# Kernel tuning notes

Measured on AMD Instinct MI355X. Metric: run time of the kernel, lower is better.

Reference implementation:

```python
import jax, jax.numpy as jnp
import numpy as np

MAX_WORDS = 256  # = batch['labels'].shape[1]


def _align(hidden, word_ids, max_words):
    """Batched segment-mean: (B,S,D) subtoken states -> (B,max_words,D) word states.
    Equivalent to align_subtokens_to_words applied per sample (word_ids all valid)."""
    B, S, D = hidden.shape
    seg = (word_ids.astype(jnp.int32) + jnp.arange(B, dtype=jnp.int32)[:, None] * max_words).reshape(-1)
    sums = jax.ops.segment_sum(hidden.reshape(-1, D), seg, num_segments=B * max_words)
    cnts = jax.ops.segment_sum(jnp.ones((B * S,), hidden.dtype), seg, num_segments=B * max_words)
    out = jnp.where(cnts[:, None] > 0, sums / jnp.maximum(cnts, 1.0)[:, None], 0.0)
    return out.reshape(B, max_words, D)


def setup_inputs() -> dict:
    key = jax.random.key(0)
    ks = jax.random.split(key, 8)
    B, S, D, W = 64, 512, 768, MAX_WORDS
    h_hing_sub = jax.random.normal(ks[0], (B, S, D), dtype=jnp.float32)
    h_rob_sub = jax.random.normal(ks[1], (B, S, D), dtype=jnp.float32)
    hing_word_ids = jnp.sort(jax.random.randint(ks[2], (B, S), 0, W), axis=-1).astype(jnp.int32)
    rob_word_ids = jnp.sort(jax.random.randint(ks[3], (B, S), 0, W), axis=-1).astype(jnp.int32)
    num_words = jax.random.randint(ks[4], (B,), 1, W).astype(jnp.int32)
    router_w1 = jax.random.normal(ks[5], (2 * D, 256), dtype=jnp.float32) * (1.0 / np.sqrt(2 * D))
    router_b1 = jnp.zeros((256,), jnp.float32)
    router_w2 = jax.random.normal(ks[6], (256, 1), dtype=jnp.float32) * (1.0 / 16.0)
    router_b2 = jnp.zeros((1,), jnp.float32)
    head_w = jax.random.normal(ks[7], (D, 7), dtype=jnp.float32) * (1.0 / np.sqrt(D))
    head_b = jnp.zeros((7,), jnp.float32)
    return {
        'h_hing_sub': h_hing_sub, 'h_rob_sub': h_rob_sub,
        'hing_word_ids': hing_word_ids, 'rob_word_ids': rob_word_ids,
        'num_words': num_words,
        'router_w1': router_w1, 'router_b1': router_b1,
        'router_w2': router_w2, 'router_b2': router_b2,
        'head_w': head_w, 'head_b': head_b,
    }


def reference(h_hing_sub, h_rob_sub, hing_word_ids, rob_word_ids, num_words,
              router_w1, router_b1, router_w2, router_b2, head_w, head_b):
    W = MAX_WORDS
    # scatter-mean subtokens -> words (the dominant custom-kernel op)
    h_hing = _align(h_hing_sub, hing_word_ids, W)   # (B, W, 768)
    h_rob = _align(h_rob_sub, rob_word_ids, W)      # (B, W, 768)
    # token-level MLP router on concatenated word states (router_input='both')
    router_in = jnp.concatenate([h_hing, h_rob], axis=-1)             # (B, W, 1536)
    hdn = jax.nn.relu(jnp.einsum('bwd,dh->bwh', router_in, router_w1) + router_b1)
    alpha = jax.nn.sigmoid(jnp.einsum('bwh,ho->bwo', hdn, router_w2) + router_b2)  # (B, W, 1)
    blended = alpha * h_hing + (1.0 - alpha) * h_rob                  # (B, W, 768)
    logits = jnp.einsum('bwd,dl->bwl', blended, head_w) + head_b      # (B, W, num_labels)
    l2_disagreement = jnp.linalg.norm(h_hing - h_rob, axis=-1)        # (B, W)
    return logits, alpha.squeeze(-1), l2_disagreement
```

## Files before the change

### kernel.cpp

```cpp
#include <hip/hip_runtime.h>
#include <hip/hip_bf16.h>
#include <math.h>

#define BATCH 64
#define SEQ   512
#define DIM   768
#define NW    256
#define NT    (BATCH * NW)
#define KDIM  1536
#define HID   256
#define NL    7

#define BM  32
#define BK  64
#define BKP 72
#define NKT (KDIM / BK)

typedef __bf16 bf16_t;
typedef bf16_t bf16x4 __attribute__((ext_vector_type(4)));
typedef bf16_t bf16x8 __attribute__((ext_vector_type(8)));
typedef float  f32x4  __attribute__((ext_vector_type(4)));

__global__ __launch_bounds__(256) void prep_kernel(
    const float* __restrict__ w1, bf16_t* __restrict__ w1t,
    const int* __restrict__ idh, const int* __restrict__ idr,
    int* __restrict__ starts)
{
    if (blockIdx.x < 192) {
        int kc = blockIdx.x >> 3;
        int kg = blockIdx.x & 7;
        int n  = threadIdx.x;
        bf16x8 v;
        #pragma unroll
        for (int j = 0; j < 8; j++)
            v[j] = (bf16_t)w1[(size_t)(kc * 64 + kg * 8 + j) * HID + n];
        *(bf16x8*)(w1t + (size_t)kc * (HID * BK) + n * BK + kg * 8) = v;
    } else {
        int blk = blockIdx.x - 192;
        int t = blk >> 6;
        int b = blk & 63;
        const int* ids = (t ? idr : idh) + b * SEQ;
        int w = threadIdx.x;
        int lo = 0, hi = SEQ;
        while (lo < hi) {
            int m = (lo + hi) >> 1;
            if (ids[m] < w) lo = m + 1; else hi = m;
        }
        int* row = starts + blk * 257;
        row[w] = lo;
        if (w == 0) row[256] = SEQ;
    }
}

__global__ __launch_bounds__(256) void align_kernel(
    const float* __restrict__ hh, const float* __restrict__ hr,
    const int* __restrict__ starts, bf16_t* __restrict__ X)
{
    int idx  = blockIdx.x * 256 + threadIdx.x;
    int rest = idx / 192;
    int c    = idx - rest * 192;
    rest     = __builtin_amdgcn_readfirstlane(rest);
    int w    = rest & 255;
    int t    = (rest >> 8) & 1;
    int b    = rest >> 9;

    const int* st = starts + (t * 64 + b) * 257;
    int lo = st[w];
    int hi = st[w + 1];

    const f32x4* src = (const f32x4*)((t ? hr : hh) + (size_t)b * SEQ * DIM);
    bf16_t*      dst = X + (size_t)b * NW * KDIM + (size_t)w * KDIM
                         + t * DIM + c * 4;

    bf16x4 o = {};
    int n = hi - lo;
    if (n > 0) {
        f32x4 acc = src[(size_t)lo * 192 + c];
        for (int s = lo + 1; s < hi; s++) {
            f32x4 v = src[(size_t)s * 192 + c];
            acc[0] += v[0]; acc[1] += v[1];
            acc[2] += v[2]; acc[3] += v[3];
        }
        float inv = 1.0f / (float)n;
        o[0] = (bf16_t)(acc[0] * inv);
        o[1] = (bf16_t)(acc[1] * inv);
        o[2] = (bf16_t)(acc[2] * inv);
        o[3] = (bf16_t)(acc[3] * inv);
    }
    *(bf16x4*)dst = o;
}

__global__ __launch_bounds__(256) void gemm_alpha_kernel(
    const bf16_t* __restrict__ X, const bf16_t* __restrict__ w1t,
    const float* __restrict__ b1, const float* __restrict__ w2,
    const float* __restrict__ b2, float* __restrict__ out)
{
    __shared__ __align__(16) bf16_t Xs[BM][BKP];
    __shared__ __align__(16) bf16_t Ws[HID][BKP];
    __shared__ float alpha_acc[BM];

    int tid   = threadIdx.x;
    int lane  = tid & 63;
    int wv    = tid >> 6;
    int row16 = lane & 15;
    int quad  = lane >> 4;
    int tok0  = blockIdx.x * BM;

    f32x4 acc[2][4];
    #pragma unroll
    for (int mi = 0; mi < 2; mi++)
        #pragma unroll
        for (int ni = 0; ni < 4; ni++)
            acc[mi][ni] = (f32x4){0.f, 0.f, 0.f, 0.f};

    int xr = tid >> 3;
    int xc = tid & 7;

    for (int kc = 0; kc < NKT; kc++) {
        {
            const uint4* src = (const uint4*)(X + (size_t)(tok0 + xr) * KDIM + kc * BK + xc * 8);
            *(uint4*)(&Xs[xr][xc * 8]) = *src;
        }
        {
            const uint4* srcb = (const uint4*)(w1t + (size_t)kc * (HID * BK));
            #pragma unroll
            for (int i = 0; i < 8; i++) {
                int cidx = tid + i * 256;
                *(uint4*)(&Ws[cidx >> 3][(cidx & 7) * 8]) = srcb[cidx];
            }
        }
        __syncthreads();
        #pragma unroll
        for (int kk2 = 0; kk2 < 2; kk2++) {
            bf16x8 af[2], bfg[4];
            #pragma unroll
            for (int mi = 0; mi < 2; mi++)
                af[mi] = *(const bf16x8*)(&Xs[mi * 16 + row16][kk2 * 32 + quad * 8]);
            #pragma unroll
            for (int ni = 0; ni < 4; ni++)
                bfg[ni] = *(const bf16x8*)(&Ws[wv * 64 + ni * 16 + row16][kk2 * 32 + quad * 8]);
            #pragma unroll
            for (int mi = 0; mi < 2; mi++)
                #pragma unroll
                for (int ni = 0; ni < 4; ni++)
                    acc[mi][ni] = __builtin_amdgcn_mfma_f32_16x16x32_bf16(
                        af[mi], bfg[ni], acc[mi][ni], 0, 0, 0);
        }
        __syncthreads();
    }

    float w2v[4], b1v[4];
    #pragma unroll
    for (int ni = 0; ni < 4; ni++) {
        int col = wv * 64 + ni * 16 + row16;
        w2v[ni] = w2[col];
        b1v[ni] = b1[col];
    }
    if (tid < BM) alpha_acc[tid] = 0.f;
    __syncthreads();

    #pragma unroll
    for (int mi = 0; mi < 2; mi++) {
        #pragma unroll
        for (int r = 0; r < 4; r++) {
            float p = 0.f;
            #pragma unroll
            for (int ni = 0; ni < 4; ni++) {
                float v = acc[mi][ni][r] + b1v[ni];
                v = v > 0.f ? v : 0.f;
                p += v * w2v[ni];
            }
            p += __shfl_xor(p, 1);
            p += __shfl_xor(p, 2);
            p += __shfl_xor(p, 4);
            p += __shfl_xor(p, 8);
            if (row16 == 0)
                atomicAdd(&alpha_acc[mi * 16 + quad * 4 + r], p);
        }
    }
    __syncthreads();
    if (tid < BM) {
        float a = 1.f / (1.f + expf(-(alpha_acc[tid] + b2[0])));
        out[(size_t)NT * NL + tok0 + tid] = a;
    }
}

__global__ __launch_bounds__(256) void blend_kernel(
    const bf16_t* __restrict__ X, const float* __restrict__ hw,
    const float* __restrict__ hb, float* __restrict__ out)
{
    __shared__ float hws[NL * DIM];
    int tid  = threadIdx.x;
    int lane = tid & 63;
    int wv   = tid >> 6;

    for (int i = tid; i < DIM * NL; i += 256) {
        int d = i / NL, l = i - d * NL;
        hws[l * DIM + d] = hw[i];
    }
    __syncthreads();

    int g   = lane >> 3;
    int u   = lane & 7;
    int tok = blockIdx.x * 32 + wv * 8 + g;

    float a = out[(size_t)NT * NL + tok];
    const bf16_t* xrow = X + (size_t)tok * KDIM;

    float lg[NL] = {0.f, 0.f, 0.f, 0.f, 0.f, 0.f, 0.f};
    float l2 = 0.f;

    #pragma unroll
    for (int k = 0; k < 12; k++) {
        int d0 = (k * 8 + u) * 8;
        bf16x8 hp = *(const bf16x8*)(xrow + d0);
        bf16x8 rp = *(const bf16x8*)(xrow + DIM + d0);
        float bl[8];
        #pragma unroll
        for (int e = 0; e < 8; e++) {
            float hhv = (float)hp[e];
            float hrv = (float)rp[e];
            float df  = hhv - hrv;
            bl[e] = fmaf(a, df, hrv);
            l2 = fmaf(df, df, l2);
        }
        #pragma unroll
        for (int l = 0; l < NL; l++) {
            f32x4 wA = *(const f32x4*)(&hws[l * DIM + d0]);
            f32x4 wB = *(const f32x4*)(&hws[l * DIM + d0 + 4]);
            lg[l] += bl[0]*wA[0] + bl[1]*wA[1] + bl[2]*wA[2] + bl[3]*wA[3]
                   + bl[4]*wB[0] + bl[5]*wB[1] + bl[6]*wB[2] + bl[7]*wB[3];
        }
    }

    #pragma unroll
    for (int off = 1; off < 8; off <<= 1) {
        #pragma unroll
        for (int l = 0; l < NL; l++) lg[l] += __shfl_xor(lg[l], off);
        l2 += __shfl_xor(l2, off);
    }

    if (u < NL) {
        float v = (u == 0) ? lg[0] : (u == 1) ? lg[1] : (u == 2) ? lg[2]
                : (u == 3) ? lg[3] : (u == 4) ? lg[4] : (u == 5) ? lg[5] : lg[6];
        out[(size_t)tok * NL + u] = v + hb[u];
    } else {
        out[(size_t)NT * NL + NT + tok] = sqrtf(l2);
    }
}

extern "C" void kernel_launch(void* const* d_in, const int* in_sizes, int n_in,
                              void* d_out, int out_size, void* d_ws, size_t ws_size,
                              hipStream_t stream)
{
    const float* hh  = (const float*)d_in[0];
    const float* hr  = (const float*)d_in[1];
    const int*   idh = (const int*)d_in[2];
    const int*   idr = (const int*)d_in[3];
    const float* w1  = (const float*)d_in[5];
    const float* b1  = (const float*)d_in[6];
    const float* w2  = (const float*)d_in[7];
    const float* b2  = (const float*)d_in[8];
    const float* hw  = (const float*)d_in[9];
    const float* hb  = (const float*)d_in[10];
    float* out = (float*)d_out;

    bf16_t* X      = (bf16_t*)d_ws;
    bf16_t* w1t    = X + (size_t)NT * KDIM;
    int*    starts = (int*)(w1t + (size_t)NKT * HID * BK);

    prep_kernel<<<320, 256, 0, stream>>>(w1, w1t, idh, idr, starts);
    align_kernel<<<24576, 256, 0, stream>>>(hh, hr, starts, X);
    gemm_alpha_kernel<<<NT / BM, 256, 0, stream>>>(X, w1t, b1, w2, b2, out);
    blend_kernel<<<512, 256, 0, stream>>>(X, hw, hb, out);
}
```

Before: 279.8 us.

## Fuse align, router GEMM and blend into one kernel with LDS-resident word states

Merges the segment-mean align, the router MLP GEMM and the blend/logits/L2 stage into a single kernel. Each 512-thread block handles 16 words of one batch row and keeps their bf16 word states in shared memory, so the intermediate X buffer no longer makes a global round trip. The GEMM now reads W1 fragments straight from global/L2 instead of staging them in LDS. In exchange there are only 1024 blocks, a 16-row MFMA tile, and the per-word 7x768 head-weight transpose is recomputed in every block, which may hurt latency hiding.

```diff
diff --git a/kernel.cpp b/kernel.cpp
--- a/kernel.cpp
+++ b/kernel.cpp
@@ -10,11 +10,12 @@
 #define KDIM  1536
 #define HID   256
 #define NL    7
-
-#define BM  32
-#define BK  64
-#define BKP 72
-#define NKT (KDIM / BK)
+#define BK    64
+#define NKT   (KDIM / BK)
+
+#define TPB   512
+#define TPW   16
+#define XSP   1544
 
 typedef __bf16 bf16_t;
 typedef bf16_t bf16x4 __attribute__((ext_vector_type(4)));
@@ -52,200 +53,148 @@
     }
 }
 
-__global__ __launch_bounds__(256) void align_kernel(
+__global__ __launch_bounds__(TPB, 4) void fused_kernel(
     const float* __restrict__ hh, const float* __restrict__ hr,
-    const int* __restrict__ starts, bf16_t* __restrict__ X)
+    const int* __restrict__ starts, const bf16_t* __restrict__ w1t,
+    const float* __restrict__ b1, const float* __restrict__ w2,
+    const float* __restrict__ b2, const float* __restrict__ hw,
+    const float* __restrict__ hb, float* __restrict__ out)
 {
-    int idx  = blockIdx.x * 256 + threadIdx.x;
-    int rest = idx / 192;
-    int c    = idx - rest * 192;
-    rest     = __builtin_amdgcn_readfirstlane(rest);
-    int w    = rest & 255;
-    int t    = (rest >> 8) & 1;
-    int b    = rest >> 9;
-
-    const int* st = starts + (t * 64 + b) * 257;
-    int lo = st[w];
-    int hi = st[w + 1];
-
-    const f32x4* src = (const f32x4*)((t ? hr : hh) + (size_t)b * SEQ * DIM);
-    bf16_t*      dst = X + (size_t)b * NW * KDIM + (size_t)w * KDIM
-                         + t * DIM + c * 4;
-
-    bf16x4 o = {};
-    int n = hi - lo;
-    if (n > 0) {
-        f32x4 acc = src[(size_t)lo * 192 + c];
-        for (int s = lo + 1; s < hi; s++) {
-            f32x4 v = src[(size_t)s * 192 + c];
-            acc[0] += v[0]; acc[1] += v[1];
-            acc[2] += v[2]; acc[3] += v[3];
-        }
-        float inv = 1.0f / (float)n;
-        o[0] = (bf16_t)(acc[0] * inv);
-        o[1] = (bf16_t)(acc[1] * inv);
-        o[2] = (bf16_t)(acc[2] * inv);
-        o[3] = (bf16_t)(acc[3] * inv);
-    }
-    *(bf16x4*)dst = o;
-}
-
-__global__ __launch_bounds__(256) void gemm_alpha_kernel(
-    const bf16_t* __restrict__ X, const bf16_t* __restrict__ w1t,
-    const float* __restrict__ b1, const float* __restrict__ w2,
-    const float* __restrict__ b2, float* __restrict__ out)
-{
-    __shared__ __align__(16) bf16_t Xs[BM][BKP];
-    __shared__ __align__(16) bf16_t Ws[HID][BKP];
-    __shared__ float alpha_acc[BM];
-
-    int tid   = threadIdx.x;
-    int lane  = tid & 63;
-    int wv    = tid >> 6;
+    __shared__ __align__(16) bf16_t Xs[TPW][XSP];
+    __shared__ float hws[NL * DIM];
+    __shared__ float alpha_acc[TPW];
+    __shared__ float alpha_s[TPW];
+
+    int tid  = threadIdx.x;
+    int lane = tid & 63;
+    int wv   = tid >> 6;
+    int b    = blockIdx.x >> 4;
+    int wb   = blockIdx.x & 15;
+    int tok0 = b * NW + wb * TPW;
+
+    for (int i = tid; i < DIM * NL; i += TPB) {
+        int d = i / NL, l = i - d * NL;
+        hws[l * DIM + d] = hw[i];
+    }
+    if (tid < TPW) alpha_acc[tid] = 0.f;
+
+    #pragma unroll
+    for (int wi = 0; wi < 2; wi++) {
+        int wl = wv * 2 + wi;
+        int w  = wb * TPW + wl;
+        #pragma unroll
+        for (int tt = 0; tt < 2; tt++) {
+            const int* st = starts + (tt * 64 + b) * 257;
+            int lo = __builtin_amdgcn_readfirstlane(st[w]);
+            int n  = __builtin_amdgcn_readfirstlane(st[w + 1]) - lo;
+            const f32x4* src = (const f32x4*)((tt ? hr : hh)
+                                + (size_t)b * SEQ * DIM) + lane;
+            f32x4 a0 = {0.f,0.f,0.f,0.f}, a1 = a0, a2 = a0;
+            for (int s = lo; s < lo + n; s++) {
+                const f32x4* r = src + (size_t)s * 192;
+                a0 += r[0]; a1 += r[64]; a2 += r[128];
+            }
+            float inv = n > 0 ? 1.0f / (float)n : 0.0f;
+            bf16x4 o0, o1, o2;
+            #pragma unroll
+            for (int e = 0; e < 4; e++) {
+                o0[e] = (bf16_t)(a0[e] * inv);
+                o1[e] = (bf16_t)(a1[e] * inv);
+                o2[e] = (bf16_t)(a2[e] * inv);
+            }
+            bf16_t* xr = &Xs[wl][tt * DIM];
+            *(bf16x4*)(xr + lane * 4)         = o0;
+            *(bf16x4*)(xr + (lane + 64) * 4)  = o1;
+            *(bf16x4*)(xr + (lane + 128) * 4) = o2;
+        }
+    }
+    __syncthreads();
+
     int row16 = lane & 15;
     int quad  = lane >> 4;
-    int tok0  = blockIdx.x * BM;
-
-    f32x4 acc[2][4];
-    #pragma unroll
-    for (int mi = 0; mi < 2; mi++)
-        #pragma unroll
-        for (int ni = 0; ni < 4; ni++)
-            acc[mi][ni] = (f32x4){0.f, 0.f, 0.f, 0.f};
-
-    int xr = tid >> 3;
-    int xc = tid & 7;
-
-    for (int kc = 0; kc < NKT; kc++) {
-        {
-            const uint4* src = (const uint4*)(X + (size_t)(tok0 + xr) * KDIM + kc * BK + xc * 8);
-            *(uint4*)(&Xs[xr][xc * 8]) = *src;
-        }
-        {
-            const uint4* srcb = (const uint4*)(w1t + (size_t)kc * (HID * BK));
-            #pragma unroll
-            for (int i = 0; i < 8; i++) {
-                int cidx = tid + i * 256;
-                *(uint4*)(&Ws[cidx >> 3][(cidx & 7) * 8]) = srcb[cidx];
-            }
-        }
-        __syncthreads();
-        #pragma unroll
-        for (int kk2 = 0; kk2 < 2; kk2++) {
-            bf16x8 af[2], bfg[4];
-            #pragma unroll
-            for (int mi = 0; mi < 2; mi++)
-                af[mi] = *(const bf16x8*)(&Xs[mi * 16 + row16][kk2 * 32 + quad * 8]);
-            #pragma unroll
-            for (int ni = 0; ni < 4; ni++)
-                bfg[ni] = *(const bf16x8*)(&Ws[wv * 64 + ni * 16 + row16][kk2 * 32 + quad * 8]);
-            #pragma unroll
-            for (int mi = 0; mi < 2; mi++)
-                #pragma unroll
-                for (int ni = 0; ni < 4; ni++)
-                    acc[mi][ni] = __builtin_amdgcn_mfma_f32_16x16x32_bf16(
-                        af[mi], bfg[ni], acc[mi][ni], 0, 0, 0);
-        }
-        __syncthreads();
-    }
-
-    float w2v[4], b1v[4];
-    #pragma unroll
-    for (int ni = 0; ni < 4; ni++) {
-        int col = wv * 64 + ni * 16 + row16;
-        w2v[ni] = w2[col];
-        b1v[ni] = b1[col];
-    }
-    if (tid < BM) alpha_acc[tid] = 0.f;
-    __syncthreads();
-
-    #pragma unroll
-    for (int mi = 0; mi < 2; mi++) {
+    f32x4 acc0 = {0.f,0.f,0.f,0.f}, acc1 = acc0;
+    int col0 = wv * 32 + row16;
+    #pragma unroll 2
+    for (int ks = 0; ks < 48; ks++) {
+        int kc = ks >> 1, k2 = ks & 1;
+        bf16x8 af = *(const bf16x8*)(&Xs[row16][ks * 32 + quad * 8]);
+        const bf16_t* bp = w1t + (size_t)kc * (HID * BK) + k2 * 32 + quad * 8;
+        bf16x8 bf0 = *(const bf16x8*)(bp + (size_t)col0 * BK);
+        bf16x8 bf1 = *(const bf16x8*)(bp + (size_t)(col0 + 16) * BK);
+        acc0 = __builtin_amdgcn_mfma_f32_16x16x32_bf16(af, bf0, acc0, 0, 0, 0);
+        acc1 = __builtin_amdgcn_mfma_f32_16x16x32_bf16(af, bf1, acc1, 0, 0, 0);
+    }
+
+    {
+        float w2v0 = w2[col0],     b1v0 = b1[col0];
+        float w2v1 = w2[col0 + 16], b1v1 = b1[col0 + 16];
         #pragma unroll
         for (int r = 0; r < 4; r++) {
-            float p = 0.f;
-            #pragma unroll
-            for (int ni = 0; ni < 4; ni++) {
-                float v = acc[mi][ni][r] + b1v[ni];
-                v = v > 0.f ? v : 0.f;
-                p += v * w2v[ni];
-            }
+            float v0 = acc0[r] + b1v0; v0 = v0 > 0.f ? v0 : 0.f;
+            float v1 = acc1[r] + b1v1; v1 = v1 > 0.f ? v1 : 0.f;
+            float p = v0 * w2v0 + v1 * w2v1;
             p += __shfl_xor(p, 1);
             p += __shfl_xor(p, 2);
             p += __shfl_xor(p, 4);
             p += __shfl_xor(p, 8);
             if (row16 == 0)
-                atomicAdd(&alpha_acc[mi * 16 + quad * 4 + r], p);
+                atomicAdd(&alpha_acc[quad * 4 + r], p);
         }
     }
     __syncthreads();
-    if (tid < BM) {
+    if (tid < TPW) {
         float a = 1.f / (1.f + expf(-(alpha_acc[tid] + b2[0])));
+        alpha_s[tid] = a;
         out[(size_t)NT * NL + tok0 + tid] = a;
     }
-}
-
-__global__ __launch_bounds__(256) void blend_kernel(
-    const bf16_t* __restrict__ X, const float* __restrict__ hw,
-    const float* __restrict__ hb, float* __restrict__ out)
-{
-    __shared__ float hws[NL * DIM];
-    int tid  = threadIdx.x;
-    int lane = tid & 63;
-    int wv   = tid >> 6;
-
-    for (int i = tid; i < DIM * NL; i += 256) {
-        int d = i / NL, l = i - d * NL;
-        hws[l * DIM + d] = hw[i];
-    }
     __syncthreads();
 
-    int g   = lane >> 3;
-    int u   = lane & 7;
-    int tok = blockIdx.x * 32 + wv * 8 + g;
-
-    float a = out[(size_t)NT * NL + tok];
-    const bf16_t* xrow = X + (size_t)tok * KDIM;
-
-    float lg[NL] = {0.f, 0.f, 0.f, 0.f, 0.f, 0.f, 0.f};
-    float l2 = 0.f;
-
-    #pragma unroll
-    for (int k = 0; k < 12; k++) {
-        int d0 = (k * 8 + u) * 8;
-        bf16x8 hp = *(const bf16x8*)(xrow + d0);
-        bf16x8 rp = *(const bf16x8*)(xrow + DIM + d0);
-        float bl[8];
-        #pragma unroll
-        for (int e = 0; e < 8; e++) {
-            float hhv = (float)hp[e];
-            float hrv = (float)rp[e];
-            float df  = hhv - hrv;
-            bl[e] = fmaf(a, df, hrv);
-            l2 = fmaf(df, df, l2);
-        }
-        #pragma unroll
-        for (int l = 0; l < NL; l++) {
-            f32x4 wA = *(const f32x4*)(&hws[l * DIM + d0]);
-            f32x4 wB = *(const f32x4*)(&hws[l * DIM + d0 + 4]);
-            lg[l] += bl[0]*wA[0] + bl[1]*wA[1] + bl[2]*wA[2] + bl[3]*wA[3]
-                   + bl[4]*wB[0] + bl[5]*wB[1] + bl[6]*wB[2] + bl[7]*wB[3];
-        }
-    }
-
-    #pragma unroll
-    for (int off = 1; off < 8; off <<= 1) {
-        #pragma unroll
-        for (int l = 0; l < NL; l++) lg[l] += __shfl_xor(lg[l], off);
-        l2 += __shfl_xor(l2, off);
-    }
-
-    if (u < NL) {
-        float v = (u == 0) ? lg[0] : (u == 1) ? lg[1] : (u == 2) ? lg[2]
-                : (u == 3) ? lg[3] : (u == 4) ? lg[4] : (u == 5) ? lg[5] : lg[6];
-        out[(size_t)tok * NL + u] = v + hb[u];
-    } else {
-        out[(size_t)NT * NL + NT + tok] = sqrtf(l2);
+    {
+        int tl = wv * 2 + (lane >> 5);
+        int u  = lane & 31;
+        float a = alpha_s[tl];
+
+        float lg[NL] = {0.f, 0.f, 0.f, 0.f, 0.f, 0.f, 0.f};
+        float l2 = 0.f;
+
+        #pragma unroll
+        for (int g3 = 0; g3 < 3; g3++) {
+            int d0 = u * 24 + g3 * 8;
+            bf16x8 hp = *(const bf16x8*)(&Xs[tl][d0]);
+            bf16x8 rp = *(const bf16x8*)(&Xs[tl][DIM + d0]);
+            float bl[8];
+            #pragma unroll
+            for (int e = 0; e < 8; e++) {
+                float hhv = (float)hp[e];
+                float hrv = (float)rp[e];
+                float df  = hhv - hrv;
+                bl[e] = fmaf(a, df, hrv);
+                l2 = fmaf(df, df, l2);
+            }
+            #pragma unroll
+            for (int l = 0; l < NL; l++) {
+                f32x4 wA = *(const f32x4*)(&hws[l * DIM + d0]);
+                f32x4 wB = *(const f32x4*)(&hws[l * DIM + d0 + 4]);
+                lg[l] += bl[0]*wA[0] + bl[1]*wA[1] + bl[2]*wA[2] + bl[3]*wA[3]
+                       + bl[4]*wB[0] + bl[5]*wB[1] + bl[6]*wB[2] + bl[7]*wB[3];
+            }
+        }
+
+        #pragma unroll
+        for (int off = 1; off < 32; off <<= 1) {
+            #pragma unroll
+            for (int l = 0; l < NL; l++) lg[l] += __shfl_xor(lg[l], off);
+            l2 += __shfl_xor(l2, off);
+        }
+
+        int tok = tok0 + tl;
+        if (u < NL) {
+            float v = (u == 0) ? lg[0] : (u == 1) ? lg[1] : (u == 2) ? lg[2]
+                    : (u == 3) ? lg[3] : (u == 4) ? lg[4] : (u == 5) ? lg[5] : lg[6];
+            out[(size_t)tok * NL + u] = v + hb[u];
+        } else if (u == NL) {
+            out[(size_t)NT * NL + NT + tok] = sqrtf(l2);
+        }
     }
 }
 
@@ -265,12 +214,10 @@
     const float* hb  = (const float*)d_in[10];
     float* out = (float*)d_out;
 
-    bf16_t* X      = (bf16_t*)d_ws;
-    bf16_t* w1t    = X + (size_t)NT * KDIM;
+    bf16_t* w1t    = (bf16_t*)d_ws;
     int*    starts = (int*)(w1t + (size_t)NKT * HID * BK);
 
     prep_kernel<<<320, 256, 0, stream>>>(w1, w1t, idh, idr, starts);
-    align_kernel<<<24576, 256, 0, stream>>>(hh, hr, starts, X);
-    gemm_alpha_kernel<<<NT / BM, 256, 0, stream>>>(X, w1t, b1, w2, b2, out);
-    blend_kernel<<<512, 256, 0, stream>>>(X, hw, hb, out);
+    fused_kernel<<<BATCH * 16, TPB, 0, stream>>>(hh, hr, starts, w1t,
+                                                 b1, w2, b2, hw, hb, out);
 }
```

After: 335.3 us. 19.8% more time.

## Fuse blend into GEMM epilogue and give each wave one word in align

Applied to the files above, without the earlier changes.

The blend/logits/L2 kernel is merged into the router GEMM kernel. It reuses the weight-tile shared memory for the head weights and keeps alpha in shared memory, which removes one launch and the global round-trip of alpha. The align kernel is restructured so each wavefront handles one (batch, type, word) row, with three f32x4 accumulators per lane and wave-uniform segment bounds. This replaces the earlier per-thread division indexing and cuts the block count. The extra smem staging of the head weights adds latency to the GEMM tail.

```diff
diff --git a/kernel.cpp b/kernel.cpp
--- a/kernel.cpp
+++ b/kernel.cpp
@@ -56,48 +56,55 @@
     const float* __restrict__ hh, const float* __restrict__ hr,
     const int* __restrict__ starts, bf16_t* __restrict__ X)
 {
-    int idx  = blockIdx.x * 256 + threadIdx.x;
-    int rest = idx / 192;
-    int c    = idx - rest * 192;
-    rest     = __builtin_amdgcn_readfirstlane(rest);
-    int w    = rest & 255;
-    int t    = (rest >> 8) & 1;
-    int b    = rest >> 9;
+    int tid  = threadIdx.x;
+    int lane = tid & 63;
+    int wv   = tid >> 6;
+    int task = blockIdx.x * 4 + wv;
+    int w    = task & 255;
+    int t    = (task >> 8) & 1;
+    int b    = task >> 9;
 
     const int* st = starts + (t * 64 + b) * 257;
-    int lo = st[w];
-    int hi = st[w + 1];
-
-    const f32x4* src = (const f32x4*)((t ? hr : hh) + (size_t)b * SEQ * DIM);
-    bf16_t*      dst = X + (size_t)b * NW * KDIM + (size_t)w * KDIM
-                         + t * DIM + c * 4;
-
-    bf16x4 o = {};
-    int n = hi - lo;
-    if (n > 0) {
-        f32x4 acc = src[(size_t)lo * 192 + c];
-        for (int s = lo + 1; s < hi; s++) {
-            f32x4 v = src[(size_t)s * 192 + c];
-            acc[0] += v[0]; acc[1] += v[1];
-            acc[2] += v[2]; acc[3] += v[3];
-        }
-        float inv = 1.0f / (float)n;
-        o[0] = (bf16_t)(acc[0] * inv);
-        o[1] = (bf16_t)(acc[1] * inv);
-        o[2] = (bf16_t)(acc[2] * inv);
-        o[3] = (bf16_t)(acc[3] * inv);
-    }
-    *(bf16x4*)dst = o;
-}
-
-__global__ __launch_bounds__(256) void gemm_alpha_kernel(
+    int lo = __builtin_amdgcn_readfirstlane(st[w]);
+    int hi = __builtin_amdgcn_readfirstlane(st[w + 1]);
+    int n  = hi - lo;
+
+    const f32x4* src = (const f32x4*)((t ? hr : hh) + (size_t)b * SEQ * DIM) + lane;
+    bf16_t*      xr  = X + (size_t)b * NW * KDIM + (size_t)w * KDIM + t * DIM;
+
+    f32x4 a0 = {0.f,0.f,0.f,0.f}, a1 = a0, a2 = a0;
+    for (int s = lo; s < hi; s++) {
+        const f32x4* r = src + (size_t)s * 192;
+        f32x4 v0 = r[0];
+        f32x4 v1 = r[64];
+        f32x4 v2 = r[128];
+        a0 += v0; a1 += v1; a2 += v2;
+    }
+    float inv = n > 0 ? 1.0f / (float)n : 0.0f;
+    bf16x4 o0, o1, o2;
+    #pragma unroll
+    for (int e = 0; e < 4; e++) {
+        o0[e] = (bf16_t)(a0[e] * inv);
+        o1[e] = (bf16_t)(a1[e] * inv);
+        o2[e] = (bf16_t)(a2[e] * inv);
+    }
+    *(bf16x4*)(xr + lane * 4)         = o0;
+    *(bf16x4*)(xr + (lane + 64) * 4)  = o1;
+    *(bf16x4*)(xr + (lane + 128) * 4) = o2;
+}
+
+__global__ __launch_bounds__(256) void gemm_blend_kernel(
     const bf16_t* __restrict__ X, const bf16_t* __restrict__ w1t,
     const float* __restrict__ b1, const float* __restrict__ w2,
-    const float* __restrict__ b2, float* __restrict__ out)
-{
-    __shared__ __align__(16) bf16_t Xs[BM][BKP];
-    __shared__ __align__(16) bf16_t Ws[HID][BKP];
+    const float* __restrict__ b2, const float* __restrict__ hw,
+    const float* __restrict__ hb, float* __restrict__ out)
+{
+    __shared__ __align__(16) unsigned char smem[4608 + 36864];
+    bf16_t (*Xs)[BKP] = (bf16_t (*)[BKP])smem;
+    bf16_t (*Ws)[BKP] = (bf16_t (*)[BKP])(smem + 4608);
+    float*  hws       = (float*)(smem + 4608);
     __shared__ float alpha_acc[BM];
+    __shared__ float alpha_s[BM];
 
     int tid   = threadIdx.x;
     int lane  = tid & 63;
@@ -178,21 +185,6 @@
                 atomicAdd(&alpha_acc[mi * 16 + quad * 4 + r], p);
         }
     }
-    __syncthreads();
-    if (tid < BM) {
-        float a = 1.f / (1.f + expf(-(alpha_acc[tid] + b2[0])));
-        out[(size_t)NT * NL + tok0 + tid] = a;
-    }
-}
-
-__global__ __launch_bounds__(256) void blend_kernel(
-    const bf16_t* __restrict__ X, const float* __restrict__ hw,
-    const float* __restrict__ hb, float* __restrict__ out)
-{
-    __shared__ float hws[NL * DIM];
-    int tid  = threadIdx.x;
-    int lane = tid & 63;
-    int wv   = tid >> 6;
 
     for (int i = tid; i < DIM * NL; i += 256) {
         int d = i / NL, l = i - d * NL;
@@ -200,52 +192,61 @@
     }
     __syncthreads();
 
-    int g   = lane >> 3;
-    int u   = lane & 7;
-    int tok = blockIdx.x * 32 + wv * 8 + g;
-
-    float a = out[(size_t)NT * NL + tok];
-    const bf16_t* xrow = X + (size_t)tok * KDIM;
-
-    float lg[NL] = {0.f, 0.f, 0.f, 0.f, 0.f, 0.f, 0.f};
-    float l2 = 0.f;
-
-    #pragma unroll
-    for (int k = 0; k < 12; k++) {
-        int d0 = (k * 8 + u) * 8;
-        bf16x8 hp = *(const bf16x8*)(xrow + d0);
-        bf16x8 rp = *(const bf16x8*)(xrow + DIM + d0);
-        float bl[8];
-        #pragma unroll
-        for (int e = 0; e < 8; e++) {
-            float hhv = (float)hp[e];
-            float hrv = (float)rp[e];
-            float df  = hhv - hrv;
-            bl[e] = fmaf(a, df, hrv);
-            l2 = fmaf(df, df, l2);
-        }
-        #pragma unroll
-        for (int l = 0; l < NL; l++) {
-            f32x4 wA = *(const f32x4*)(&hws[l * DIM + d0]);
-            f32x4 wB = *(const f32x4*)(&hws[l * DIM + d0 + 4]);
-            lg[l] += bl[0]*wA[0] + bl[1]*wA[1] + bl[2]*wA[2] + bl[3]*wA[3]
-                   + bl[4]*wB[0] + bl[5]*wB[1] + bl[6]*wB[2] + bl[7]*wB[3];
-        }
-    }
-
-    #pragma unroll
-    for (int off = 1; off < 8; off <<= 1) {
-        #pragma unroll
-        for (int l = 0; l < NL; l++) lg[l] += __shfl_xor(lg[l], off);
-        l2 += __shfl_xor(l2, off);
-    }
-
-    if (u < NL) {
-        float v = (u == 0) ? lg[0] : (u == 1) ? lg[1] : (u == 2) ? lg[2]
-                : (u == 3) ? lg[3] : (u == 4) ? lg[4] : (u == 5) ? lg[5] : lg[6];
-        out[(size_t)tok * NL + u] = v + hb[u];
-    } else {
-        out[(size_t)NT * NL + NT + tok] = sqrtf(l2);
+    if (tid < BM) {
+        float a = 1.f / (1.f + expf(-(alpha_acc[tid] + b2[0])));
+        alpha_s[tid] = a;
+        out[(size_t)NT * NL + tok0 + tid] = a;
+    }
+    __syncthreads();
+
+    {
+        int g   = lane >> 3;
+        int u   = lane & 7;
+        int tl  = wv * 8 + g;
+        int tok = tok0 + tl;
+        float a = alpha_s[tl];
+        const bf16_t* xrow = X + (size_t)tok * KDIM;
+
+        float lg[NL] = {0.f, 0.f, 0.f, 0.f, 0.f, 0.f, 0.f};
+        float l2 = 0.f;
+
+        #pragma unroll
+        for (int k = 0; k < 12; k++) {
+            int d0 = (k * 8 + u) * 8;
+            bf16x8 hp = *(const bf16x8*)(xrow + d0);
+            bf16x8 rp = *(const bf16x8*)(xrow + DIM + d0);
+            float bl[8];
+            #pragma unroll
+            for (int e = 0; e < 8; e++) {
+                float hhv = (float)hp[e];
+                float hrv = (float)rp[e];
+                float df  = hhv - hrv;
+                bl[e] = fmaf(a, df, hrv);
+                l2 = fmaf(df, df, l2);
+            }
+            #pragma unroll
+            for (int l = 0; l < NL; l++) {
+                f32x4 wA = *(const f32x4*)(&hws[l * DIM + d0]);
+                f32x4 wB = *(const f32x4*)(&hws[l * DIM + d0 + 4]);
+                lg[l] += bl[0]*wA[0] + bl[1]*wA[1] + bl[2]*wA[2] + bl[3]*wA[3]
+                       + bl[4]*wB[0] + bl[5]*wB[1] + bl[6]*wB[2] + bl[7]*wB[3];
+            }
+        }
+
+        #pragma unroll
+        for (int off = 1; off < 8; off <<= 1) {
+            #pragma unroll
+            for (int l = 0; l < NL; l++) lg[l] += __shfl_xor(lg[l], off);
+            l2 += __shfl_xor(l2, off);
+        }
+
+        if (u < NL) {
+            float v = (u == 0) ? lg[0] : (u == 1) ? lg[1] : (u == 2) ? lg[2]
+                    : (u == 3) ? lg[3] : (u == 4) ? lg[4] : (u == 5) ? lg[5] : lg[6];
+            out[(size_t)tok * NL + u] = v + hb[u];
+        } else {
+            out[(size_t)NT * NL + NT + tok] = sqrtf(l2);
+        }
     }
 }
 
@@ -270,7 +271,7 @@
     int*    starts = (int*)(w1t + (size_t)NKT * HID * BK);
 
     prep_kernel<<<320, 256, 0, stream>>>(w1, w1t, idh, idr, starts);
-    align_kernel<<<24576, 256, 0, stream>>>(hh, hr, starts, X);
-    gemm_alpha_kernel<<<NT / BM, 256, 0, stream>>>(X, w1t, b1, w2, b2, out);
-    blend_kernel<<<512, 256, 0, stream>>>(X, hw, hb, out);
-}
+    align_kernel<<<8192, 256, 0, stream>>>(hh, hr, starts, X);
+    gemm_blend_kernel<<<NT / BM, 256, 0, stream>>>(X, w1t, b1, w2, b2,
+                                                   hw, hb, out);
+}
```

New measurement: 283.6 us. About the same (+1.3%).
